# Optimization experiments

Hardware: AMD Instinct MI355X
Metric: run time of the kernel (lower is better)

Reference implementation:

```python
import jax, jax.numpy as jnp
import numpy as np

B, T, H, DH = 4, 2048, 16, 128
D = H * DH            # inner_dim = 2048
F = 4096              # mlp_inner_dim
E = 8                 # num_expert_mlp
TOP_K = 2


def setup_inputs() -> dict:
    key = jax.random.key(0)
    ks = jax.random.split(key, 5)
    s_in = 1.0 / np.sqrt(D)
    s_f = 1.0 / np.sqrt(F)
    return {
        "stm": jax.random.normal(ks[0], (B, T, H, DH), dtype=jnp.float32),
        "gate_w": jax.random.normal(ks[1], (E, D), dtype=jnp.float32) * s_in,
        "w1": jax.random.normal(ks[2], (E, F, D), dtype=jnp.float32) * s_in,
        "w2": jax.random.normal(ks[3], (E, D, F), dtype=jnp.float32) * s_f,
        "w3": jax.random.normal(ks[4], (E, F, D), dtype=jnp.float32) * s_in,
    }


def reference(stm, gate_w, w1, w2, w3):
    b, t, h, dh = stm.shape
    d = h * dh
    x = stm.reshape(b * t, d)                                   # [N, D]
    logits = x @ gate_w.T                                       # [N, E]
    top_logit, top_idx = jax.lax.top_k(logits, TOP_K)           # [N, 2]
    gw = jax.nn.softmax(top_logit.astype(jnp.float32), axis=1).astype(x.dtype)
    out = jnp.zeros_like(x)
    n_expert = w1.shape[0]
    for e in range(n_expert):
        # combine weight for expert e per token (0 if not routed)
        we = jnp.sum(jnp.where(top_idx == e, gw, jnp.zeros_like(gw)), axis=1)  # [N]
        gate = jax.nn.silu(x @ w1[e].T)                          # [N, F]
        up = x @ w3[e].T                                         # [N, F]
        y = (gate * up) @ w2[e].T                                # [N, D]
        out = out + we[:, None] * y
    return out.reshape(b, t, h, dh)
```

## Files before the change

kernel.cpp:

```cpp
#include <hip/hip_runtime.h>
#include <hip/hip_bf16.h>
#include <stdint.h>

#define N_TOK 8192
#define DIM   2048
#define FDIM  4096
#define NEXP  8

#define XB_OFF   0ull
#define HB_OFF   33554432ull
#define WB1_OFF  176160768ull
#define WB3_OFF  243269632ull
#define META_OFF 310378496ull
#define CNT_OFF   (META_OFF)
#define EBASE_OFF (META_OFF + 64ull)
#define ELIST_OFF (META_OFF + 128ull)
#define EWTS_OFF  (ELIST_OFF + 262144ull)

typedef float f32x4 __attribute__((ext_vector_type(4)));
typedef short s16x8 __attribute__((ext_vector_type(8)));

__device__ __forceinline__ uint32_t pkbf(float a, float b) {
  uint32_t ua = __builtin_bit_cast(uint32_t, a) + 0x8000u;
  uint32_t ub = __builtin_bit_cast(uint32_t, b) + 0x8000u;
  return (ua >> 16) | (ub & 0xffff0000u);
}

__device__ __forceinline__ void gld16(const void* g, void* l) {
  __builtin_amdgcn_global_load_lds(
      (__attribute__((address_space(1))) void*)g,
      (__attribute__((address_space(3))) void*)l, 16, 0, 0);
}

__global__ void zero_out_k(float* out) {
  const size_t i = ((size_t)blockIdx.x * 256 + threadIdx.x) * 4;
  *(float4*)(out + i) = make_float4(0.f, 0.f, 0.f, 0.f);
}

__global__ void init_k(int* cnt) {
  if (threadIdx.x < NEXP) cnt[threadIdx.x] = 0;
}

__global__ void router_k(const float* __restrict__ x, const float* __restrict__ gw,
                         __hip_bfloat16* __restrict__ xb, int* __restrict__ cnt,
                         int* __restrict__ elist, float* __restrict__ ewts) {
  const int n = blockIdx.x;
  const int t = threadIdx.x;
  const float* xr = x + (size_t)n * DIM;
  const float4 v0 = *(const float4*)(xr + t * 8);
  const float4 v1 = *(const float4*)(xr + t * 8 + 4);
  uint4 u;
  u.x = pkbf(v0.x, v0.y); u.y = pkbf(v0.z, v0.w);
  u.z = pkbf(v1.x, v1.y); u.w = pkbf(v1.z, v1.w);
  *(uint4*)(xb + (size_t)n * DIM + t * 8) = u;

  float p[NEXP];
#pragma unroll
  for (int e = 0; e < NEXP; ++e) {
    const float* g = gw + e * DIM + t * 8;
    const float4 g0 = *(const float4*)g;
    const float4 g1 = *(const float4*)(g + 4);
    p[e] = v0.x * g0.x + v0.y * g0.y + v0.z * g0.z + v0.w * g0.w +
           v1.x * g1.x + v1.y * g1.y + v1.z * g1.z + v1.w * g1.w;
  }
#pragma unroll
  for (int off = 32; off >= 1; off >>= 1)
#pragma unroll
    for (int e = 0; e < NEXP; ++e) p[e] += __shfl_xor(p[e], off, 64);

  __shared__ float red[4][NEXP];
  const int lane = t & 63, wv = t >> 6;
  if (lane == 0) {
#pragma unroll
    for (int e = 0; e < NEXP; ++e) red[wv][e] = p[e];
  }
  __syncthreads();
  if (t == 0) {
    float l0 = -1e30f, l1 = -1e30f;
    int e0 = 0, e1 = 0;
#pragma unroll
    for (int e = 0; e < NEXP; ++e) {
      float v = red[0][e] + red[1][e] + red[2][e] + red[3][e];
      if (v > l0) { l1 = l0; e1 = e0; l0 = v; e0 = e; }
      else if (v > l1) { l1 = v; e1 = e; }
    }
    const float ed = expf(l1 - l0);
    const float inv = 1.f / (1.f + ed);
    int s0 = atomicAdd(cnt + e0, 1);
    elist[e0 * N_TOK + s0] = n;
    ewts[e0 * N_TOK + s0] = inv;
    int s1 = atomicAdd(cnt + e1, 1);
    elist[e1 * N_TOK + s1] = (int)((uint32_t)n | 0x80000000u);
    ewts[e1 * N_TOK + s1] = ed * inv;
  }
}

__global__ void scan_k(const int* __restrict__ cnt, int* __restrict__ ebase) {
  if (threadIdx.x == 0 && blockIdx.x == 0) {
    int b = 0;
    for (int e = 0; e < NEXP; ++e) { ebase[e] = b; b += (cnt[e] + 127) & ~127; }
  }
}

__global__ void convW_k(const float* __restrict__ src, __hip_bfloat16* __restrict__ dst,
                        int r0, int nrh, int rtot, int kd) {
  const int cpr = kd / 8;
  const int total = NEXP * nrh * cpr;
  for (int i = blockIdx.x * blockDim.x + threadIdx.x; i < total;
       i += gridDim.x * blockDim.x) {
    const int e = i / (nrh * cpr);
    const int rem = i - e * nrh * cpr;
    const int lr = rem / cpr;
    const int c = rem - lr * cpr;
    const float* s = src + ((size_t)e * rtot + r0 + lr) * (size_t)kd + c * 8;
    const float4 a = *(const float4*)s;
    const float4 b = *(const float4*)(s + 4);
    uint4 u;
    u.x = pkbf(a.x, a.y); u.y = pkbf(a.z, a.w);
    u.z = pkbf(b.x, b.y); u.w = pkbf(b.z, b.w);
    *(uint4*)(dst + ((size_t)e * nrh + lr) * (size_t)kd + c * 8) = u;
  }
}

__global__ __launch_bounds__(256, 2) void moe_up_k(
    const __hip_bfloat16* __restrict__ xb, const __hip_bfloat16* __restrict__ w1b,
    const __hip_bfloat16* __restrict__ w3b, __hip_bfloat16* __restrict__ hb,
    const int* __restrict__ cnt, const int* __restrict__ ebase,
    const int* __restrict__ elist, int noff) {
  const int e = blockIdx.z;
  const int count = cnt[e];
  const int mt = blockIdx.y;
  if (mt * 128 >= count) return;
  const int bn0 = blockIdx.x * 128;
  const int ncol0 = noff + bn0;

  __shared__ char lds[49152];
  const int t = threadIdx.x;
  const int lane = t & 63, wv = t >> 6;
  const int wr = wv >> 1, wc = wv & 1;
  const int* lst = elist + e * N_TOK;
  const size_t hrow0 = (size_t)ebase[e] + (size_t)mt * 128;

  const int r0 = t >> 2;
  const int ks = (t & 3) ^ ((r0 >> 1) & 3);
  size_t sA[2], sB1[2], sB3[2];
  int ldsO[2];
#pragma unroll
  for (int i = 0; i < 2; ++i) {
    const int r = r0 + i * 64;
    int idx = mt * 128 + r;
    if (idx >= count) idx = 0;
    const size_t tok = (size_t)(lst[idx] & 0x7fffffff);
    sA[i] = tok * DIM + ks * 8;
    sB1[i] = ((size_t)e * 2048 + bn0 + r) * DIM + ks * 8;
    sB3[i] = sB1[i];
    ldsO[i] = i * 4096 + wv * 1024;
  }

  const int fr = lane & 15;
  const int swzc = ((lane >> 4) ^ ((fr >> 1) & 3)) << 4;
  const int aoff = (wr * 64 + fr) * 64 + swzc;
  const int boff = (wc * 64 + fr) * 64 + swzc;

  f32x4 accG[4][4], accU[4][4];
#pragma unroll
  for (int mi = 0; mi < 4; ++mi)
#pragma unroll
    for (int ni = 0; ni < 4; ++ni) {
      accG[mi][ni] = {0.f, 0.f, 0.f, 0.f};
      accU[mi][ni] = {0.f, 0.f, 0.f, 0.f};
    }

  auto stage = [&](int k0, int b) {
#pragma unroll
    for (int i = 0; i < 2; ++i)
      gld16(xb + sA[i] + k0, lds + b * 8192 + ldsO[i]);
#pragma unroll
    for (int i = 0; i < 2; ++i)
      gld16(w1b + sB1[i] + k0, lds + 16384 + b * 8192 + ldsO[i]);
#pragma unroll
    for (int i = 0; i < 2; ++i)
      gld16(w3b + sB3[i] + k0, lds + 32768 + b * 8192 + ldsO[i]);
  };

  stage(0, 0);
  __syncthreads();

  int b = 0;
  for (int kt = 0; kt < DIM / 32; ++kt) {
    const int nk = (kt + 1) * 32;
    if (nk < DIM) stage(nk, b ^ 1);
    s16x8 af[4], b1f[4], b3f[4];
#pragma unroll
    for (int mi = 0; mi < 4; ++mi)
      af[mi] = *(const s16x8*)(lds + b * 8192 + aoff + mi * 1024);
#pragma unroll
    for (int ni = 0; ni < 4; ++ni) {
      b1f[ni] = *(const s16x8*)(lds + 16384 + b * 8192 + boff + ni * 1024);
      b3f[ni] = *(const s16x8*)(lds + 32768 + b * 8192 + boff + ni * 1024);
    }
#pragma unroll
    for (int mi = 0; mi < 4; ++mi)
#pragma unroll
      for (int ni = 0; ni < 4; ++ni) {
        accG[mi][ni] = __builtin_amdgcn_mfma_f32_16x16x32_bf16(
            af[mi], b1f[ni], accG[mi][ni], 0, 0, 0);
        accU[mi][ni] = __builtin_amdgcn_mfma_f32_16x16x32_bf16(
            af[mi], b3f[ni], accU[mi][ni], 0, 0, 0);
      }
    __syncthreads();
    b ^= 1;
  }

  const int erow = (lane >> 4) * 4;
  const int ecol = lane & 15;
#pragma unroll
  for (int mi = 0; mi < 4; ++mi)
#pragma unroll
    for (int ni = 0; ni < 4; ++ni) {
      const size_t cb = ncol0 + wc * 64 + ni * 16 + ecol;
#pragma unroll
      for (int j = 0; j < 4; ++j) {
        const size_t r = hrow0 + wr * 64 + mi * 16 + erow + j;
        const float g = accG[mi][ni][j];
        const float uu = accU[mi][ni][j];
        const float h = g / (1.f + __expf(-g)) * uu;
        hb[r * FDIM + cb] = __float2bfloat16(h);
      }
    }
}

__global__ __launch_bounds__(256, 2) void moe_down_k(
    const __hip_bfloat16* __restrict__ hb, const __hip_bfloat16* __restrict__ w2b,
    float* __restrict__ out, const int* __restrict__ cnt,
    const int* __restrict__ ebase, const int* __restrict__ elist,
    const float* __restrict__ ewts, int noff) {
  const int e = blockIdx.z;
  const int count = cnt[e];
  const int mt = blockIdx.y;
  if (mt * 128 >= count) return;
  const int bn0 = blockIdx.x * 128;
  const int ncol0 = noff + bn0;

  __shared__ char lds[32768];
  const int t = threadIdx.x;
  const int lane = t & 63, wv = t >> 6;
  const int wr = wv >> 1, wc = wv & 1;
  const int* lst = elist + e * N_TOK;
  const size_t hrow0 = (size_t)ebase[e] + (size_t)mt * 128;

  const int r0 = t >> 2;
  const int ks = (t & 3) ^ ((r0 >> 1) & 3);
  size_t sA[2], sB[2];
  int ldsO[2];
#pragma unroll
  for (int i = 0; i < 2; ++i) {
    const int r = r0 + i * 64;
    sA[i] = (hrow0 + r) * (size_t)FDIM + ks * 8;
    sB[i] = ((size_t)e * 1024 + bn0 + r) * (size_t)FDIM + ks * 8;
    ldsO[i] = i * 4096 + wv * 1024;
  }

  const int fr = lane & 15;
  const int swzc = ((lane >> 4) ^ ((fr >> 1) & 3)) << 4;
  const int aoff = (wr * 64 + fr) * 64 + swzc;
  const int boff = 16384 + (wc * 64 + fr) * 64 + swzc;

  f32x4 acc[4][4];
#pragma unroll
  for (int mi = 0; mi < 4; ++mi)
#pragma unroll
    for (int ni = 0; ni < 4; ++ni) acc[mi][ni] = {0.f, 0.f, 0.f, 0.f};

  auto stage = [&](int k0, int b) {
#pragma unroll
    for (int i = 0; i < 2; ++i)
      gld16(hb + sA[i] + k0, lds + b * 8192 + ldsO[i]);
#pragma unroll
    for (int i = 0; i < 2; ++i)
      gld16(w2b + sB[i] + k0, lds + 16384 + b * 8192 + ldsO[i]);
  };

  stage(0, 0);
  __syncthreads();

  int b = 0;
  for (int kt = 0; kt < FDIM / 32; ++kt) {
    const int nk = (kt + 1) * 32;
    if (nk < FDIM) stage(nk, b ^ 1);
    s16x8 af[4], bf[4];
#pragma unroll
    for (int mi = 0; mi < 4; ++mi)
      af[mi] = *(const s16x8*)(lds + b * 8192 + aoff + mi * 1024);
#pragma unroll
    for (int ni = 0; ni < 4; ++ni)
      bf[ni] = *(const s16x8*)(lds + b * 8192 + boff + ni * 1024);
#pragma unroll
    for (int mi = 0; mi < 4; ++mi)
#pragma unroll
      for (int ni = 0; ni < 4; ++ni)
        acc[mi][ni] = __builtin_amdgcn_mfma_f32_16x16x32_bf16(
            af[mi], bf[ni], acc[mi][ni], 0, 0, 0);
    __syncthreads();
    b ^= 1;
  }

  const int erow = (lane >> 4) * 4;
  const int ecol = lane & 15;
#pragma unroll
  for (int mi = 0; mi < 4; ++mi)
#pragma unroll
    for (int j = 0; j < 4; ++j) {
      const int i = mt * 128 + wr * 64 + mi * 16 + erow + j;
      if (i < count) {
        const uint32_t info = (uint32_t)lst[i];
        const int tok = (int)(info & 0x7fffffffu);
        const float wt = ewts[e * N_TOK + i];
        float* prow = out + (size_t)tok * DIM;
#pragma unroll
        for (int ni = 0; ni < 4; ++ni) {
          const int cb = ncol0 + wc * 64 + ni * 16 + ecol;
          atomicAdd(prow + cb, wt * acc[mi][ni][j]);
        }
      }
    }
}

extern "C" void kernel_launch(void* const* d_in, const int* in_sizes, int n_in,
                              void* d_out, int out_size, void* d_ws, size_t ws_size,
                              hipStream_t stream) {
  const float* stm = (const float*)d_in[0];
  const float* gw = (const float*)d_in[1];
  const float* w1 = (const float*)d_in[2];
  const float* w2 = (const float*)d_in[3];
  const float* w3 = (const float*)d_in[4];
  float* out = (float*)d_out;
  char* ws = (char*)d_ws;

  __hip_bfloat16* xb = (__hip_bfloat16*)(ws + XB_OFF);
  __hip_bfloat16* hb = (__hip_bfloat16*)(ws + HB_OFF);
  __hip_bfloat16* wb1 = (__hip_bfloat16*)(ws + WB1_OFF);
  __hip_bfloat16* wb3 = (__hip_bfloat16*)(ws + WB3_OFF);
  int* cnt = (int*)(ws + CNT_OFF);
  int* ebase = (int*)(ws + EBASE_OFF);
  int* elist = (int*)(ws + ELIST_OFF);
  float* ewts = (float*)(ws + EWTS_OFF);

  zero_out_k<<<N_TOK * DIM / 1024, 256, 0, stream>>>(out);
  init_k<<<1, 64, 0, stream>>>(cnt);
  router_k<<<N_TOK, 256, 0, stream>>>(stm, gw, xb, cnt, elist, ewts);
  scan_k<<<1, 64, 0, stream>>>(cnt, ebase);

  const dim3 gUp(16, 64, 8);
  const dim3 gDn(8, 64, 8);

  convW_k<<<2048, 256, 0, stream>>>(w1, wb1, 0, 2048, FDIM, DIM);
  convW_k<<<2048, 256, 0, stream>>>(w3, wb3, 0, 2048, FDIM, DIM);
  moe_up_k<<<gUp, 256, 0, stream>>>(xb, wb1, wb3, hb, cnt, ebase, elist, 0);
  convW_k<<<2048, 256, 0, stream>>>(w1, wb1, 2048, 2048, FDIM, DIM);
  convW_k<<<2048, 256, 0, stream>>>(w3, wb3, 2048, 2048, FDIM, DIM);
  moe_up_k<<<gUp, 256, 0, stream>>>(xb, wb1, wb3, hb, cnt, ebase, elist, 2048);

  convW_k<<<2048, 256, 0, stream>>>(w2, wb1, 0, 1024, DIM, FDIM);
  moe_down_k<<<gDn, 256, 0, stream>>>(hb, wb1, out, cnt, ebase, elist, ewts, 0);
  convW_k<<<2048, 256, 0, stream>>>(w2, wb1, 1024, 1024, DIM, FDIM);
  moe_down_k<<<gDn, 256, 0, stream>>>(hb, wb1, out, cnt, ebase, elist, ewts, 1024);
}
```

Baseline: 1.595 ms.

## Replace atomic scatter-add with per-slot partial buffers and a combine pass

The down-projection no longer zeroes the output and atomically adds into it. Each token's two routed contributions are written with plain stores into a per-slot partial buffer that reuses the w3 workspace, and a combine kernel sums the two slots into the output for each column half. This removes the zero-fill pass and contended float atomics, at the cost of an extra read/write pass over the partials. It also raises the launch-bounds occupancy hint from 2 to 3 for both GEMMs and drops a redundant address array. It relies on the routing list's high bit encoding the slot, and on every token filling both slots.

```diff
diff --git a/kernel.cpp b/kernel.cpp
--- a/kernel.cpp
+++ b/kernel.cpp
@@ -30,11 +30,6 @@
   __builtin_amdgcn_global_load_lds(
       (__attribute__((address_space(1))) void*)g,
       (__attribute__((address_space(3))) void*)l, 16, 0, 0);
-}
-
-__global__ void zero_out_k(float* out) {
-  const size_t i = ((size_t)blockIdx.x * 256 + threadIdx.x) * 4;
-  *(float4*)(out + i) = make_float4(0.f, 0.f, 0.f, 0.f);
 }
 
 __global__ void init_k(int* cnt) {
@@ -122,7 +117,19 @@
   }
 }
 
-__global__ __launch_bounds__(256, 2) void moe_up_k(
+__global__ void combine_k(const float* __restrict__ part, float* __restrict__ out,
+                          int noff) {
+  const size_t i4 = (size_t)blockIdx.x * 256 + threadIdx.x;
+  const int tok = (int)(i4 >> 8);
+  const int c = (int)(i4 & 255) * 4;
+  const float4 a = *(const float4*)(part + ((size_t)tok) * 1024 + c);
+  const float4 b = *(const float4*)(part + ((size_t)N_TOK + tok) * 1024 + c);
+  float4 o;
+  o.x = a.x + b.x; o.y = a.y + b.y; o.z = a.z + b.z; o.w = a.w + b.w;
+  *(float4*)(out + (size_t)tok * DIM + noff + c) = o;
+}
+
+__global__ __launch_bounds__(256, 3) void moe_up_k(
     const __hip_bfloat16* __restrict__ xb, const __hip_bfloat16* __restrict__ w1b,
     const __hip_bfloat16* __restrict__ w3b, __hip_bfloat16* __restrict__ hb,
     const int* __restrict__ cnt, const int* __restrict__ ebase,
@@ -143,7 +150,7 @@
 
   const int r0 = t >> 2;
   const int ks = (t & 3) ^ ((r0 >> 1) & 3);
-  size_t sA[2], sB1[2], sB3[2];
+  size_t sA[2], sB1[2];
   int ldsO[2];
 #pragma unroll
   for (int i = 0; i < 2; ++i) {
@@ -153,7 +160,6 @@
     const size_t tok = (size_t)(lst[idx] & 0x7fffffff);
     sA[i] = tok * DIM + ks * 8;
     sB1[i] = ((size_t)e * 2048 + bn0 + r) * DIM + ks * 8;
-    sB3[i] = sB1[i];
     ldsO[i] = i * 4096 + wv * 1024;
   }
 
@@ -180,7 +186,7 @@
       gld16(w1b + sB1[i] + k0, lds + 16384 + b * 8192 + ldsO[i]);
 #pragma unroll
     for (int i = 0; i < 2; ++i)
-      gld16(w3b + sB3[i] + k0, lds + 32768 + b * 8192 + ldsO[i]);
+      gld16(w3b + sB1[i] + k0, lds + 32768 + b * 8192 + ldsO[i]);
   };
 
   stage(0, 0);
@@ -230,17 +236,16 @@
     }
 }
 
-__global__ __launch_bounds__(256, 2) void moe_down_k(
+__global__ __launch_bounds__(256, 3) void moe_down_k(
     const __hip_bfloat16* __restrict__ hb, const __hip_bfloat16* __restrict__ w2b,
-    float* __restrict__ out, const int* __restrict__ cnt,
+    float* __restrict__ part, const int* __restrict__ cnt,
     const int* __restrict__ ebase, const int* __restrict__ elist,
-    const float* __restrict__ ewts, int noff) {
+    const float* __restrict__ ewts) {
   const int e = blockIdx.z;
   const int count = cnt[e];
   const int mt = blockIdx.y;
   if (mt * 128 >= count) return;
   const int bn0 = blockIdx.x * 128;
-  const int ncol0 = noff + bn0;
 
   __shared__ char lds[32768];
   const int t = threadIdx.x;
@@ -315,12 +320,13 @@
       if (i < count) {
         const uint32_t info = (uint32_t)lst[i];
         const int tok = (int)(info & 0x7fffffffu);
+        const int slot = (int)(info >> 31);
         const float wt = ewts[e * N_TOK + i];
-        float* prow = out + (size_t)tok * DIM;
+        float* prow = part + ((size_t)slot * N_TOK + tok) * 1024;
 #pragma unroll
         for (int ni = 0; ni < 4; ++ni) {
-          const int cb = ncol0 + wc * 64 + ni * 16 + ecol;
-          atomicAdd(prow + cb, wt * acc[mi][ni][j]);
+          const int cb = bn0 + wc * 64 + ni * 16 + ecol;
+          prow[cb] = wt * acc[mi][ni][j];
         }
       }
     }
@@ -341,12 +347,12 @@
   __hip_bfloat16* hb = (__hip_bfloat16*)(ws + HB_OFF);
   __hip_bfloat16* wb1 = (__hip_bfloat16*)(ws + WB1_OFF);
   __hip_bfloat16* wb3 = (__hip_bfloat16*)(ws + WB3_OFF);
+  float* part = (float*)(ws + WB3_OFF);
   int* cnt = (int*)(ws + CNT_OFF);
   int* ebase = (int*)(ws + EBASE_OFF);
   int* elist = (int*)(ws + ELIST_OFF);
   float* ewts = (float*)(ws + EWTS_OFF);
 
-  zero_out_k<<<N_TOK * DIM / 1024, 256, 0, stream>>>(out);
   init_k<<<1, 64, 0, stream>>>(cnt);
   router_k<<<N_TOK, 256, 0, stream>>>(stm, gw, xb, cnt, elist, ewts);
   scan_k<<<1, 64, 0, stream>>>(cnt, ebase);
@@ -362,7 +368,9 @@
   moe_up_k<<<gUp, 256, 0, stream>>>(xb, wb1, wb3, hb, cnt, ebase, elist, 2048);
 
   convW_k<<<2048, 256, 0, stream>>>(w2, wb1, 0, 1024, DIM, FDIM);
-  moe_down_k<<<gDn, 256, 0, stream>>>(hb, wb1, out, cnt, ebase, elist, ewts, 0);
+  moe_down_k<<<gDn, 256, 0, stream>>>(hb, wb1, part, cnt, ebase, elist, ewts);
+  combine_k<<<8192, 256, 0, stream>>>(part, out, 0);
   convW_k<<<2048, 256, 0, stream>>>(w2, wb1, 1024, 1024, DIM, FDIM);
-  moe_down_k<<<gDn, 256, 0, stream>>>(hb, wb1, out, cnt, ebase, elist, ewts, 1024);
-}
+  moe_down_k<<<gDn, 256, 0, stream>>>(hb, wb1, part, cnt, ebase, elist, ewts);
+  combine_k<<<8192, 256, 0, stream>>>(part, out, 1024);
+}
```

New measurement: 1.891 ms. 18.5% more time.

## Widen down-projection tile to 128x256 and convert all of W2 in one pass

Applied to the files above, without the earlier changes.

The down-projection kernel now computes two 128-column output halves per block, sharing each loaded tile of the hidden activations across both. This lets one launch cover the full 2048 output columns instead of two. W2 is converted to bf16 in a single launch into a larger workspace region, replacing two conversion/GEMM pairs. Hidden activations are read from memory half as often and launch count drops, at the cost of twice the accumulator registers and more LDS per block, which may lower occupancy.

```diff
diff --git a/kernel.cpp b/kernel.cpp
--- a/kernel.cpp
+++ b/kernel.cpp
@@ -143,7 +143,7 @@
 
   const int r0 = t >> 2;
   const int ks = (t & 3) ^ ((r0 >> 1) & 3);
-  size_t sA[2], sB1[2], sB3[2];
+  size_t sA[2], sB1[2];
   int ldsO[2];
 #pragma unroll
   for (int i = 0; i < 2; ++i) {
@@ -153,7 +153,6 @@
     const size_t tok = (size_t)(lst[idx] & 0x7fffffff);
     sA[i] = tok * DIM + ks * 8;
     sB1[i] = ((size_t)e * 2048 + bn0 + r) * DIM + ks * 8;
-    sB3[i] = sB1[i];
     ldsO[i] = i * 4096 + wv * 1024;
   }
 
@@ -180,7 +179,7 @@
       gld16(w1b + sB1[i] + k0, lds + 16384 + b * 8192 + ldsO[i]);
 #pragma unroll
     for (int i = 0; i < 2; ++i)
-      gld16(w3b + sB3[i] + k0, lds + 32768 + b * 8192 + ldsO[i]);
+      gld16(w3b + sB1[i] + k0, lds + 32768 + b * 8192 + ldsO[i]);
   };
 
   stage(0, 0);
@@ -234,15 +233,14 @@
     const __hip_bfloat16* __restrict__ hb, const __hip_bfloat16* __restrict__ w2b,
     float* __restrict__ out, const int* __restrict__ cnt,
     const int* __restrict__ ebase, const int* __restrict__ elist,
-    const float* __restrict__ ewts, int noff) {
+    const float* __restrict__ ewts) {
   const int e = blockIdx.z;
   const int count = cnt[e];
   const int mt = blockIdx.y;
   if (mt * 128 >= count) return;
-  const int bn0 = blockIdx.x * 128;
-  const int ncol0 = noff + bn0;
-
-  __shared__ char lds[32768];
+  const int bn0 = blockIdx.x * 256;
+
+  __shared__ char lds[49152];
   const int t = threadIdx.x;
   const int lane = t & 63, wv = t >> 6;
   const int wr = wv >> 1, wc = wv & 1;
@@ -257,20 +255,23 @@
   for (int i = 0; i < 2; ++i) {
     const int r = r0 + i * 64;
     sA[i] = (hrow0 + r) * (size_t)FDIM + ks * 8;
-    sB[i] = ((size_t)e * 1024 + bn0 + r) * (size_t)FDIM + ks * 8;
+    sB[i] = ((size_t)e * 2048 + bn0 + r) * (size_t)FDIM + ks * 8;
     ldsO[i] = i * 4096 + wv * 1024;
   }
+  const size_t sBp = 128 * (size_t)FDIM;
 
   const int fr = lane & 15;
   const int swzc = ((lane >> 4) ^ ((fr >> 1) & 3)) << 4;
   const int aoff = (wr * 64 + fr) * 64 + swzc;
-  const int boff = 16384 + (wc * 64 + fr) * 64 + swzc;
-
-  f32x4 acc[4][4];
-#pragma unroll
-  for (int mi = 0; mi < 4; ++mi)
-#pragma unroll
-    for (int ni = 0; ni < 4; ++ni) acc[mi][ni] = {0.f, 0.f, 0.f, 0.f};
+  const int boff = (wc * 64 + fr) * 64 + swzc;
+
+  f32x4 accP[2][4][4];
+#pragma unroll
+  for (int p = 0; p < 2; ++p)
+#pragma unroll
+    for (int mi = 0; mi < 4; ++mi)
+#pragma unroll
+      for (int ni = 0; ni < 4; ++ni) accP[p][mi][ni] = {0.f, 0.f, 0.f, 0.f};
 
   auto stage = [&](int k0, int b) {
 #pragma unroll
@@ -279,6 +280,9 @@
 #pragma unroll
     for (int i = 0; i < 2; ++i)
       gld16(w2b + sB[i] + k0, lds + 16384 + b * 8192 + ldsO[i]);
+#pragma unroll
+    for (int i = 0; i < 2; ++i)
+      gld16(w2b + sB[i] + sBp + k0, lds + 32768 + b * 8192 + ldsO[i]);
   };
 
   stage(0, 0);
@@ -288,19 +292,24 @@
   for (int kt = 0; kt < FDIM / 32; ++kt) {
     const int nk = (kt + 1) * 32;
     if (nk < FDIM) stage(nk, b ^ 1);
-    s16x8 af[4], bf[4];
+    s16x8 af[4], b0f[4], b1f[4];
 #pragma unroll
     for (int mi = 0; mi < 4; ++mi)
       af[mi] = *(const s16x8*)(lds + b * 8192 + aoff + mi * 1024);
 #pragma unroll
-    for (int ni = 0; ni < 4; ++ni)
-      bf[ni] = *(const s16x8*)(lds + b * 8192 + boff + ni * 1024);
-#pragma unroll
-    for (int mi = 0; mi < 4; ++mi)
-#pragma unroll
-      for (int ni = 0; ni < 4; ++ni)
-        acc[mi][ni] = __builtin_amdgcn_mfma_f32_16x16x32_bf16(
-            af[mi], bf[ni], acc[mi][ni], 0, 0, 0);
+    for (int ni = 0; ni < 4; ++ni) {
+      b0f[ni] = *(const s16x8*)(lds + 16384 + b * 8192 + boff + ni * 1024);
+      b1f[ni] = *(const s16x8*)(lds + 32768 + b * 8192 + boff + ni * 1024);
+    }
+#pragma unroll
+    for (int mi = 0; mi < 4; ++mi)
+#pragma unroll
+      for (int ni = 0; ni < 4; ++ni) {
+        accP[0][mi][ni] = __builtin_amdgcn_mfma_f32_16x16x32_bf16(
+            af[mi], b0f[ni], accP[0][mi][ni], 0, 0, 0);
+        accP[1][mi][ni] = __builtin_amdgcn_mfma_f32_16x16x32_bf16(
+            af[mi], b1f[ni], accP[1][mi][ni], 0, 0, 0);
+      }
     __syncthreads();
     b ^= 1;
   }
@@ -318,10 +327,12 @@
         const float wt = ewts[e * N_TOK + i];
         float* prow = out + (size_t)tok * DIM;
 #pragma unroll
-        for (int ni = 0; ni < 4; ++ni) {
-          const int cb = ncol0 + wc * 64 + ni * 16 + ecol;
-          atomicAdd(prow + cb, wt * acc[mi][ni][j]);
-        }
+        for (int p = 0; p < 2; ++p)
+#pragma unroll
+          for (int ni = 0; ni < 4; ++ni) {
+            const int cb = bn0 + p * 128 + wc * 64 + ni * 16 + ecol;
+            atomicAdd(prow + cb, wt * accP[p][mi][ni][j]);
+          }
       }
     }
 }
@@ -341,15 +352,16 @@
   __hip_bfloat16* hb = (__hip_bfloat16*)(ws + HB_OFF);
   __hip_bfloat16* wb1 = (__hip_bfloat16*)(ws + WB1_OFF);
   __hip_bfloat16* wb3 = (__hip_bfloat16*)(ws + WB3_OFF);
+  __hip_bfloat16* w2full = (__hip_bfloat16*)(ws + WB1_OFF);
   int* cnt = (int*)(ws + CNT_OFF);
   int* ebase = (int*)(ws + EBASE_OFF);
   int* elist = (int*)(ws + ELIST_OFF);
   float* ewts = (float*)(ws + EWTS_OFF);
 
-  zero_out_k<<<N_TOK * DIM / 1024, 256, 0, stream>>>(out);
   init_k<<<1, 64, 0, stream>>>(cnt);
   router_k<<<N_TOK, 256, 0, stream>>>(stm, gw, xb, cnt, elist, ewts);
   scan_k<<<1, 64, 0, stream>>>(cnt, ebase);
+  zero_out_k<<<N_TOK * DIM / 1024, 256, 0, stream>>>(out);
 
   const dim3 gUp(16, 64, 8);
   const dim3 gDn(8, 64, 8);
@@ -361,8 +373,6 @@
   convW_k<<<2048, 256, 0, stream>>>(w3, wb3, 2048, 2048, FDIM, DIM);
   moe_up_k<<<gUp, 256, 0, stream>>>(xb, wb1, wb3, hb, cnt, ebase, elist, 2048);
 
-  convW_k<<<2048, 256, 0, stream>>>(w2, wb1, 0, 1024, DIM, FDIM);
-  moe_down_k<<<gDn, 256, 0, stream>>>(hb, wb1, out, cnt, ebase, elist, ewts, 0);
-  convW_k<<<2048, 256, 0, stream>>>(w2, wb1, 1024, 1024, DIM, FDIM);
-  moe_down_k<<<gDn, 256, 0, stream>>>(hb, wb1, out, cnt, ebase, elist, ewts, 1024);
-}
+  convW_k<<<4096, 256, 0, stream>>>(w2, w2full, 0, 2048, DIM, FDIM);
+  moe_down_k<<<gDn, 256, 0, stream>>>(hb, w2full, out, cnt, ebase, elist, ewts);
+}
```

Result: faster. 1.428 ms (-10.5%).
